# Optimization experiments

Hardware: AMD Instinct MI355X
Metric: run time of the kernel (lower is better)

The kernel has to match this reference:

```python
import jax, jax.numpy as jnp
import numpy as np
from jax import lax

N, S, C, D1, D2, P = 16384, 4096, 3, 256, 256, 16
MLP = [256, 256]
IN_CH = D1 + D2
K = 3
BIG = 1e8
EPS = 1e-8
BN_EPS = 1e-5


def setup_inputs() -> dict:
    key = jax.random.key(0)
    ks = jax.random.split(key, 16)
    inp = {
        'xyz1': jax.random.normal(ks[0], (1, C, N), jnp.float32),
        'xyz2': jax.random.normal(ks[1], (1, C, S), jnp.float32),
        'piece_id1': jax.random.randint(ks[2], (1, 1, N), 0, P, jnp.int64),
        'piece_id2': jax.random.randint(ks[3], (1, 1, S), 0, P, jnp.int64),
        'points1': jax.random.normal(ks[4], (1, D1, N), jnp.float32),
        'points2': jax.random.normal(ks[5], (1, D2, S), jnp.float32),
    }
    last = IN_CH
    for i, out in enumerate(MLP):
        inp[f'w{i}'] = jax.random.normal(ks[6 + 2 * i], (out, last), jnp.float32) / np.sqrt(last)
        inp[f'b{i}'] = jnp.zeros((out,), jnp.float32)
        inp[f'g{i}'] = jnp.ones((out,), jnp.float32)
        inp[f'bt{i}'] = jnp.zeros((out,), jnp.float32)
        last = out
    return inp


def _interpolate(xyz1, xyz2, pid1, pid2, points2):
    # xyz1 [1,3,N], xyz2 [1,3,S], pid [1,1,N]/[1,1,S], points2 [1,D,S]
    p1 = xyz1[0].T          # [N,3]
    p2 = xyz2[0].T          # [S,3]
    id1 = pid1[0, 0]        # [N]
    id2 = pid2[0, 0]        # [S]
    # squared euclidean distances, masked to same-piece neighbors (knn with batch vectors)
    d = jnp.sum((p1[:, None, :] - p2[None, :, :]) ** 2, axis=-1)  # [N,S]
    d = jnp.where(id1[:, None] != id2[None, :], jnp.inf, d)
    neg_d3, idx = lax.top_k(-d, K)    # 3 nearest per query
    d3 = -neg_d3                      # [N,3]
    valid = jnp.isfinite(d3)
    # missing neighbors -> reuse first idx with huge distance (fill_value semantics)
    idx = jnp.where(valid, idx, idx[:, :1])
    d3 = jnp.where(valid, d3, BIG)
    w = 1.0 / (d3 + EPS)
    w = w / jnp.sum(w, axis=-1, keepdims=True)   # [N,3]
    f2 = points2[0].T                            # [S,D2]
    interp = jnp.sum(f2[idx] * w[..., None], axis=1)  # [N,D2]
    return interp


def reference(xyz1, xyz2, piece_id1, piece_id2, points1, points2,
              w0, b0, g0, bt0, w1, b1, g1, bt1):
    interp = _interpolate(xyz1, xyz2, piece_id1, piece_id2, points2)  # [N,D2]
    feats = jnp.concatenate([points1[0].T, interp], axis=-1)          # [N,Cin]
    x = feats.T[None]                                                  # [1,Cin,N]
    for (wc, bc, g, bt) in ((w0, b0, g0, bt0), (w1, b1, g1, bt1)):
        y = jnp.einsum('oc,bcn->bon', wc, x) + bc[None, :, None]
        mean = jnp.mean(y, axis=(0, 2), keepdims=True)
        var = jnp.mean((y - mean) ** 2, axis=(0, 2), keepdims=True)
        y = (y - mean) * lax.rsqrt(var + BN_EPS)
        y = y * g[None, :, None] + bt[None, :, None]
        x = jax.nn.relu(y)
    return x
```

## Files before the change

### kernel.cpp

```cpp
#include <hip/hip_runtime.h>
#include <math.h>

#define NQ 16384
#define NS 4096
#define NCH 256
#define NP 16
#define BIGD 1e8f
#define EPSW 1e-8f

typedef __attribute__((ext_vector_type(8))) short short8;
typedef __attribute__((ext_vector_type(4))) float f32x4;

static __device__ __forceinline__ unsigned short f2bf(float x) {
    unsigned u = __float_as_uint(x);
    unsigned r = (u + 0x7fff + ((u >> 16) & 1)) >> 16;
    return (unsigned short)r;
}
static __device__ __forceinline__ float bf2f(unsigned short u) {
    return __uint_as_float(((unsigned)u) << 16);
}

__global__ __launch_bounds__(1024)
void bucket_kernel(const float* __restrict__ xyz2, const int* __restrict__ pid2,
                   float4* __restrict__ bpts, int* __restrict__ boff,
                   float* __restrict__ sums)
{
    __shared__ int spid[NS];
    __shared__ int segcnt[64][NP];
    __shared__ int segbase[64][NP];
    __shared__ int poff[NP + 1];
    const int t = threadIdx.x;
    sums[t] = 0.f;
    for (int i = t; i < NS; i += 1024) spid[i] = pid2[i];
    __syncthreads();
    {
        const int seg = t >> 4, p = t & 15;
        int c = 0;
        const int b = seg * 64;
        for (int i = 0; i < 64; ++i) c += (spid[b + i] == p);
        segcnt[seg][p] = c;
    }
    __syncthreads();
    if (t < NP) {
        int run = 0;
        for (int s = 0; s < 64; ++s) { segbase[s][t] = run; run += segcnt[s][t]; }
        poff[t] = run;
    }
    __syncthreads();
    if (t == 0) {
        int run = 0;
        for (int p = 0; p < NP; ++p) { int c = poff[p]; poff[p] = run; run += c; }
        poff[NP] = run;
    }
    __syncthreads();
    if (t <= NP) boff[t] = poff[t];
    {
        const int seg = t >> 4, p = t & 15;
        int pos = poff[p] + segbase[seg][p];
        const int b = seg * 64;
        for (int i = 0; i < 64; ++i) {
            const int gi = b + i;
            if (spid[gi] == p) {
                bpts[pos] = make_float4(xyz2[gi], xyz2[NS + gi], xyz2[2 * NS + gi],
                                        __int_as_float(gi));
                ++pos;
            }
        }
    }
}

#define LEXLT(d, j, e, je) ((d) < (e) || ((d) == (e) && (j) < (je)))

__global__ __launch_bounds__(256)
void knn_kernel(const float* __restrict__ xyz1, const int* __restrict__ pid1,
                const float4* __restrict__ bpts, const int* __restrict__ boff,
                int* __restrict__ oidx, float* __restrict__ ow)
{
    const int t = blockIdx.x * 256 + threadIdx.x;
    const int q = t >> 4;
    const int k = t & 15;
    const float qx = xyz1[q], qy = xyz1[NQ + q], qz = xyz1[2 * NQ + q];
    const int p = pid1[q];
    const int s0 = boff[p], s1 = boff[p + 1];

    float e0 = INFINITY, e1 = INFINITY, e2 = INFINITY;
    int j0 = 0, j1 = 0, j2 = 0;
    for (int i = s0 + k; i < s1; i += 16) {
        float4 pt = bpts[i];
        const float dx = pt.x - qx, dy = pt.y - qy, dz = pt.z - qz;
        const float d = fmaf(dx, dx, fmaf(dy, dy, dz * dz));
        const int oi = __float_as_int(pt.w);
        const bool b0 = LEXLT(d, oi, e0, j0), b1 = LEXLT(d, oi, e1, j1),
                   b2 = LEXLT(d, oi, e2, j2);
        e2 = b2 ? (b1 ? e1 : d) : e2;  j2 = b2 ? (b1 ? j1 : oi) : j2;
        e1 = b1 ? (b0 ? e0 : d) : e1;  j1 = b1 ? (b0 ? j0 : oi) : j1;
        e0 = b0 ? d : e0;              j0 = b0 ? oi : j0;
    }
    #pragma unroll
    for (int m = 1; m <= 8; m <<= 1) {
        float f[3]; int gi[3];
        f[0] = __shfl_xor(e0, m); gi[0] = __shfl_xor(j0, m);
        f[1] = __shfl_xor(e1, m); gi[1] = __shfl_xor(j1, m);
        f[2] = __shfl_xor(e2, m); gi[2] = __shfl_xor(j2, m);
        #pragma unroll
        for (int c = 0; c < 3; ++c) {
            const float d = f[c]; const int oi = gi[c];
            const bool b0 = LEXLT(d, oi, e0, j0), b1 = LEXLT(d, oi, e1, j1),
                       b2 = LEXLT(d, oi, e2, j2);
            e2 = b2 ? (b1 ? e1 : d) : e2;  j2 = b2 ? (b1 ? j1 : oi) : j2;
            e1 = b1 ? (b0 ? e0 : d) : e1;  j1 = b1 ? (b0 ? j0 : oi) : j1;
            e0 = b0 ? d : e0;              j0 = b0 ? oi : j0;
        }
    }
    if (k == 0) {
        if (isinf(e0)) { j0 = 0;  e0 = BIGD; }
        if (isinf(e1)) { j1 = j0; e1 = BIGD; }
        if (isinf(e2)) { j2 = j0; e2 = BIGD; }
        const float w0 = 1.f / (e0 + EPSW), w1 = 1.f / (e1 + EPSW), w2 = 1.f / (e2 + EPSW);
        const float inv = 1.f / (w0 + w1 + w2);
        oidx[q * 3 + 0] = j0; oidx[q * 3 + 1] = j1; oidx[q * 3 + 2] = j2;
        ow[q * 3 + 0] = w0 * inv; ow[q * 3 + 1] = w1 * inv; ow[q * 3 + 2] = w2 * inv;
    }
}

static __device__ __forceinline__
void tcvt_body(const float* __restrict__ src, int srcN,
               unsigned short* __restrict__ dst, int kt,
               int cb, int nb, float (*tile)[65])
{
    const int t = threadIdx.x;
    #pragma unroll
    for (int rnd = 0; rnd < 4; ++rnd) {
        const int r = rnd * 16 + (t >> 4);
        const int c4 = (t & 15) * 4;
        float4 v = *(const float4*)&src[(size_t)(cb + r) * srcN + nb + c4];
        tile[r][c4 + 0] = v.x; tile[r][c4 + 1] = v.y;
        tile[r][c4 + 2] = v.z; tile[r][c4 + 3] = v.w;
    }
    __syncthreads();
    #pragma unroll
    for (int half = 0; half < 2; ++half) {
        const int p  = (t >> 3) + half * 32;
        const int cg = t & 7;
        ushort4 o0, o1;
        o0.x = f2bf(tile[cg * 8 + 0][p]); o0.y = f2bf(tile[cg * 8 + 1][p]);
        o0.z = f2bf(tile[cg * 8 + 2][p]); o0.w = f2bf(tile[cg * 8 + 3][p]);
        o1.x = f2bf(tile[cg * 8 + 4][p]); o1.y = f2bf(tile[cg * 8 + 5][p]);
        o1.z = f2bf(tile[cg * 8 + 6][p]); o1.w = f2bf(tile[cg * 8 + 7][p]);
        ushort4* d = (ushort4*)&dst[(size_t)(nb + p) * kt + cb + cg * 8];
        d[0] = o0; d[1] = o1;
    }
}

static __device__ __forceinline__
void wrelay_body(const float* __restrict__ src, unsigned short* __restrict__ dst,
                 int K, int kslog, int o4)
{
    const int e4 = o4 & 1;
    const int tmp = o4 >> 1;
    const int l = tmp & 63;
    const int gks = tmp >> 6;
    const int ks = gks & ((1 << kslog) - 1);
    const int g  = gks >> kslog;
    const int row = g * 16 + (l & 15);
    const int col = ks * 32 + (l >> 4) * 8 + e4 * 4;
    float4 v = *(const float4*)&src[(size_t)row * K + col];
    ushort4 o;
    o.x = f2bf(v.x); o.y = f2bf(v.y); o.z = f2bf(v.z); o.w = f2bf(v.w);
    ((ushort4*)dst)[o4] = o;
}

__global__ __launch_bounds__(256)
void prep_kernel(const float* __restrict__ points1, const float* __restrict__ points2,
                 const float* __restrict__ w0, const float* __restrict__ w1,
                 unsigned short* __restrict__ Xt, unsigned short* __restrict__ p2Tb,
                 unsigned short* __restrict__ Wf0, unsigned short* __restrict__ Wf1)
{
    __shared__ float tile[64][65];
    const int b = blockIdx.x;
    if (b < 1024) {
        tcvt_body(points1, NQ, Xt, 512, (b & 3) * 64, (b >> 2) * 64, tile);
    } else if (b < 1280) {
        const int bb = b - 1024;
        tcvt_body(points2, NS, p2Tb, 256, (bb & 3) * 64, (bb >> 2) * 64, tile);
    } else if (b < 1408) {
        wrelay_body(w0, Wf0, 512, 4, (b - 1280) * 256 + threadIdx.x);
    } else {
        wrelay_body(w1, Wf1, 256, 3, (b - 1408) * 256 + threadIdx.x);
    }
}

__global__ __launch_bounds__(256)
void interp_kernel(const unsigned short* __restrict__ p2Tb,
                   const int* __restrict__ oidx, const float* __restrict__ ow,
                   unsigned short* __restrict__ Xt)
{
    const int n = (blockIdx.x * 256 + threadIdx.x) >> 6;
    const int l = threadIdx.x & 63;
    const int i0 = oidx[n * 3 + 0], i1 = oidx[n * 3 + 1], i2 = oidx[n * 3 + 2];
    const float w0 = ow[n * 3 + 0], w1 = ow[n * 3 + 1], w2 = ow[n * 3 + 2];
    ushort4 a = *(const ushort4*)&p2Tb[(size_t)i0 * 256 + l * 4];
    ushort4 b = *(const ushort4*)&p2Tb[(size_t)i1 * 256 + l * 4];
    ushort4 c = *(const ushort4*)&p2Tb[(size_t)i2 * 256 + l * 4];
    ushort4 o;
    o.x = f2bf(w0 * bf2f(a.x) + w1 * bf2f(b.x) + w2 * bf2f(c.x));
    o.y = f2bf(w0 * bf2f(a.y) + w1 * bf2f(b.y) + w2 * bf2f(c.y));
    o.z = f2bf(w0 * bf2f(a.z) + w1 * bf2f(b.z) + w2 * bf2f(c.z));
    o.w = f2bf(w0 * bf2f(a.w) + w1 * bf2f(b.w) + w2 * bf2f(c.w));
    *(ushort4*)&Xt[(size_t)n * 512 + 256 + l * 4] = o;
}

template<int K, bool LOAD_DIRECT>
__global__ __launch_bounds__(512)
void mgemm_kernel(const unsigned short* __restrict__ Wf,
                  const unsigned short* __restrict__ Xsrc,
                  const float* __restrict__ sum_in, const float* __restrict__ sq_in,
                  const float* __restrict__ g, const float* __restrict__ bt,
                  unsigned short* __restrict__ Yout)
{
    constexpr int K2 = K * 2;
    constexpr int KS = K / 32;
    __shared__ unsigned char sB[32 * K2];
    const int tid = threadIdx.x;
    const int n0 = blockIdx.x * 32;

    if constexpr (!LOAD_DIRECT) {
        __shared__ float scs[256], shs[256];
        if (tid < 256) {
            const float mean = sum_in[tid] * (1.f / NQ);
            const float var  = sq_in[tid] * (1.f / NQ) - mean * mean;
            const float rs = rsqrtf(var + 1e-5f);
            const float s = g[tid] * rs;
            scs[tid] = s; shs[tid] = bt[tid] - mean * s;
        }
        __syncthreads();
        const int row = tid >> 4;
        #pragma unroll
        for (int ch = 0; ch < 2; ++ch) {
            const int cb = (tid & 15) * 32 + ch * 16;
            const int c = cb / 2;
            const short8 v = *(const short8*)&Xsrc[(size_t)(n0 + row) * 256 + c];
            const float4 s0 = *(const float4*)&scs[c],     s1 = *(const float4*)&scs[c + 4];
            const float4 h0 = *(const float4*)&shs[c],     h1 = *(const float4*)&shs[c + 4];
            ushort4 lo, hi;
            lo.x = f2bf(fmaxf(fmaf(bf2f((unsigned short)v[0]), s0.x, h0.x), 0.f));
            lo.y = f2bf(fmaxf(fmaf(bf2f((unsigned short)v[1]), s0.y, h0.y), 0.f));
            lo.z = f2bf(fmaxf(fmaf(bf2f((unsigned short)v[2]), s0.z, h0.z), 0.f));
            lo.w = f2bf(fmaxf(fmaf(bf2f((unsigned short)v[3]), s0.w, h0.w), 0.f));
            hi.x = f2bf(fmaxf(fmaf(bf2f((unsigned short)v[4]), s1.x, h1.x), 0.f));
            hi.y = f2bf(fmaxf(fmaf(bf2f((unsigned short)v[5]), s1.y, h1.y), 0.f));
            hi.z = f2bf(fmaxf(fmaf(bf2f((unsigned short)v[6]), s1.z, h1.z), 0.f));
            hi.w = f2bf(fmaxf(fmaf(bf2f((unsigned short)v[7]), s1.w, h1.w), 0.f));
            unsigned char* d = &sB[row * K2 + (cb ^ ((row & 7) << 4))];
            ((ushort4*)d)[0] = lo; ((ushort4*)d)[1] = hi;
        }
    } else {
        constexpr int ROUNDS = (32 * K2 / 16) / 512;
        #pragma unroll
        for (int j = 0; j < ROUNDS; ++j) {
            const int p   = (j * 512 + tid) * 16;
            const int row = p >> 10;
            const int c   = p & (K2 - 1);
            const int q   = c ^ ((row & 7) << 4);
            const char* gp = (const char*)(Xsrc + (size_t)(n0 + row) * K) + q;
            __builtin_amdgcn_global_load_lds(
                (const __attribute__((address_space(1))) void*)gp,
                (__attribute__((address_space(3))) void*)(sB + p), 16, 0, 0);
        }
    }
    __syncthreads();

    const int w = tid >> 6, l = tid & 63;
    const int lr = l & 15, lk = l >> 4;
    f32x4 acc[2][2] = {};
    #pragma unroll
    for (int ks = 0; ks < KS; ++ks) {
        short8 b[2];
        #pragma unroll
        for (int nf = 0; nf < 2; ++nf) {
            const int r = nf * 16 + lr;
            const int cbyte = ks * 64 + lk * 16;
            b[nf] = *(const short8*)&sB[r * K2 + (cbyte ^ ((r & 7) << 4))];
        }
        #pragma unroll
        for (int mf = 0; mf < 2; ++mf) {
            const short8 a = *(const short8*)(
                Wf + (((size_t)(w * 2 + mf) * KS + ks) * 64 + l) * 8);
            #pragma unroll
            for (int nf = 0; nf < 2; ++nf)
                acc[mf][nf] = __builtin_amdgcn_mfma_f32_16x16x32_bf16(
                                  a, b[nf], acc[mf][nf], 0, 0, 0);
        }
    }
    #pragma unroll
    for (int mf = 0; mf < 2; ++mf)
        #pragma unroll
        for (int nf = 0; nf < 2; ++nf) {
            const int n = n0 + nf * 16 + lr;
            const int moff = w * 32 + mf * 16 + lk * 4;
            ushort4 o;
            o.x = f2bf(acc[mf][nf][0]); o.y = f2bf(acc[mf][nf][1]);
            o.z = f2bf(acc[mf][nf][2]); o.w = f2bf(acc[mf][nf][3]);
            *(ushort4*)&Yout[(size_t)n * 256 + moff] = o;
        }
}

__global__ __launch_bounds__(256)
void stats_kernel(const unsigned short* __restrict__ Y,
                  float* __restrict__ sum, float* __restrict__ sq)
{
    __shared__ float red[2][8][256];
    const int t = threadIdx.x;
    const int c8 = (t & 31) * 8;
    const int rsub = t >> 5;
    const int r0 = blockIdx.x * 256 + rsub;
    float s[8] = {}, q[8] = {};
    for (int i = 0; i < 32; ++i) {
        const short8 v = *(const short8*)&Y[(size_t)(r0 + i * 8) * 256 + c8];
        #pragma unroll
        for (int j = 0; j < 8; ++j) {
            const float f = bf2f((unsigned short)v[j]);
            s[j] += f; q[j] += f * f;
        }
    }
    #pragma unroll
    for (int j = 0; j < 8; ++j) {
        red[0][rsub][c8 + j] = s[j];
        red[1][rsub][c8 + j] = q[j];
    }
    __syncthreads();
    float ts = 0.f, tq = 0.f;
    #pragma unroll
    for (int r = 0; r < 8; ++r) { ts += red[0][r][t]; tq += red[1][r][t]; }
    atomicAdd(&sum[t], ts);
    atomicAdd(&sq[t], tq);
}

__global__ __launch_bounds__(256)
void bnt_kernel(const unsigned short* __restrict__ Y, const float* __restrict__ sum,
                const float* __restrict__ sq, const float* __restrict__ g,
                const float* __restrict__ bt, float* __restrict__ out)
{
    __shared__ float tile[64][65];
    __shared__ float scs[64], shs[64];
    const int t = threadIdx.x;
    const int cb = blockIdx.x * 64;
    const int nb = blockIdx.y * 64;
    if (t < 64) {
        const int c = cb + t;
        const float mean = sum[c] * (1.f / NQ);
        const float var  = sq[c] * (1.f / NQ) - mean * mean;
        const float rs = rsqrtf(var + 1e-5f);
        const float s = g[c] * rs;
        scs[t] = s; shs[t] = bt[c] - mean * s;
    }
    __syncthreads();
    #pragma unroll
    for (int rnd = 0; rnd < 4; ++rnd) {
        const int nl = rnd * 16 + (t >> 4);
        const int c4 = (t & 15) * 4;
        ushort4 v = *(const ushort4*)&Y[(size_t)(nb + nl) * 256 + cb + c4];
        tile[c4 + 0][nl] = fmaxf(fmaf(bf2f(v.x), scs[c4 + 0], shs[c4 + 0]), 0.f);
        tile[c4 + 1][nl] = fmaxf(fmaf(bf2f(v.y), scs[c4 + 1], shs[c4 + 1]), 0.f);
        tile[c4 + 2][nl] = fmaxf(fmaf(bf2f(v.z), scs[c4 + 2], shs[c4 + 2]), 0.f);
        tile[c4 + 3][nl] = fmaxf(fmaf(bf2f(v.w), scs[c4 + 3], shs[c4 + 3]), 0.f);
    }
    __syncthreads();
    const int cl = t >> 2, qq = t & 3;
    float* orow = out + (size_t)(cb + cl) * NQ + nb + qq * 16;
    #pragma unroll
    for (int k = 0; k < 4; ++k) {
        float4 v = make_float4(tile[cl][qq * 16 + k * 4 + 0], tile[cl][qq * 16 + k * 4 + 1],
                               tile[cl][qq * 16 + k * 4 + 2], tile[cl][qq * 16 + k * 4 + 3]);
        *(float4*)&orow[k * 4] = v;
    }
}

extern "C" void kernel_launch(void* const* d_in, const int* in_sizes, int n_in,
                              void* d_out, int out_size, void* d_ws, size_t ws_size,
                              hipStream_t stream)
{
    const float* xyz1    = (const float*)d_in[0];
    const float* xyz2    = (const float*)d_in[1];
    const int*   pid1    = (const int*)d_in[2];
    const int*   pid2    = (const int*)d_in[3];
    const float* points1 = (const float*)d_in[4];
    const float* points2 = (const float*)d_in[5];
    const float* w0      = (const float*)d_in[6];
    const float* g0      = (const float*)d_in[8];
    const float* bt0     = (const float*)d_in[9];
    const float* w1      = (const float*)d_in[10];
    const float* g1      = (const float*)d_in[12];
    const float* bt1     = (const float*)d_in[13];
    float* out = (float*)d_out;

    char* ws = (char*)d_ws;
    int*            boff  = (int*)(ws + 0);
    float*          sums  = (float*)(ws + 128);
    float*          sum0  = sums, *sq0 = sums + 256, *sum1 = sums + 512, *sq1 = sums + 768;
    int*            idxb  = (int*)(ws + 8192);
    float*          wb    = (float*)(ws + 8192 + 196608);
    unsigned short* Wf0   = (unsigned short*)(ws + 8192 + 393216);
    unsigned short* Wf1   = (unsigned short*)(ws + 8192 + 655360);
    float4*         bpts  = (float4*)(ws + 8192 + 786432);
    unsigned short* p2Tb  = (unsigned short*)(ws + 1048576);
    unsigned short* Xt    = (unsigned short*)(ws + 1048576 + 2097152);
    unsigned short* y0Tb  = (unsigned short*)(ws + 1048576 + 2097152 + 16777216);
    unsigned short* y1Tb  = (unsigned short*)(ws + 1048576 + 2097152 + 25165824);

    bucket_kernel<<<1, 1024, 0, stream>>>(xyz2, pid2, bpts, boff, sums);
    knn_kernel<<<NQ * 16 / 256, 256, 0, stream>>>(xyz1, pid1, bpts, boff, idxb, wb);
    prep_kernel<<<1472, 256, 0, stream>>>(points1, points2, w0, w1, Xt, p2Tb, Wf0, Wf1);
    interp_kernel<<<NQ * 64 / 256, 256, 0, stream>>>(p2Tb, idxb, wb, Xt);
    mgemm_kernel<512, true><<<NQ / 32, 512, 0, stream>>>(
        Wf0, Xt, nullptr, nullptr, nullptr, nullptr, y0Tb);
    stats_kernel<<<64, 256, 0, stream>>>(y0Tb, sum0, sq0);
    mgemm_kernel<256, false><<<NQ / 32, 512, 0, stream>>>(
        Wf1, y0Tb, sum0, sq0, g0, bt0, y1Tb);
    stats_kernel<<<64, 256, 0, stream>>>(y1Tb, sum1, sq1);
    bnt_kernel<<<dim3(4, NQ / 64), 256, 0, stream>>>(y1Tb, sum1, sq1, g1, bt1, out);
}
```

Before: 176.5 us.

## Fuse points1 transpose and interpolation into GEMM1, fold BN stats into GEMM epilogues

The first GEMM kernel now transposes and converts points1 to bf16 and computes the 3-NN weighted interpolation straight into LDS, so the Xt staging buffer and the separate interp pass are gone. Both GEMM kernels stage their output tile in swizzled LDS, write it out coalesced, and emit per-block channel sums and sums of squares. A small reduction kernel then turns these into BN scale and shift, replacing the atomic stats kernels that re-read Y. This removes several full-tensor global round trips and launches. The cost is more LDS per block and the loss of the async global-to-LDS load path in GEMM1.

```diff
diff --git a/kernel.cpp b/kernel.cpp
--- a/kernel.cpp
+++ b/kernel.cpp
@@ -3,7 +3,6 @@
 
 #define NQ 16384
 #define NS 4096
-#define NCH 256
 #define NP 16
 #define BIGD 1e8f
 #define EPSW 1e-8f
@@ -22,15 +21,13 @@
 
 __global__ __launch_bounds__(1024)
 void bucket_kernel(const float* __restrict__ xyz2, const int* __restrict__ pid2,
-                   float4* __restrict__ bpts, int* __restrict__ boff,
-                   float* __restrict__ sums)
+                   float4* __restrict__ bpts, int* __restrict__ boff)
 {
     __shared__ int spid[NS];
     __shared__ int segcnt[64][NP];
     __shared__ int segbase[64][NP];
     __shared__ int poff[NP + 1];
     const int t = threadIdx.x;
-    sums[t] = 0.f;
     for (int i = t; i < NS; i += 1024) spid[i] = pid2[i];
     __syncthreads();
     {
@@ -124,35 +121,6 @@
 }
 
 static __device__ __forceinline__
-void tcvt_body(const float* __restrict__ src, int srcN,
-               unsigned short* __restrict__ dst, int kt,
-               int cb, int nb, float (*tile)[65])
-{
-    const int t = threadIdx.x;
-    #pragma unroll
-    for (int rnd = 0; rnd < 4; ++rnd) {
-        const int r = rnd * 16 + (t >> 4);
-        const int c4 = (t & 15) * 4;
-        float4 v = *(const float4*)&src[(size_t)(cb + r) * srcN + nb + c4];
-        tile[r][c4 + 0] = v.x; tile[r][c4 + 1] = v.y;
-        tile[r][c4 + 2] = v.z; tile[r][c4 + 3] = v.w;
-    }
-    __syncthreads();
-    #pragma unroll
-    for (int half = 0; half < 2; ++half) {
-        const int p  = (t >> 3) + half * 32;
-        const int cg = t & 7;
-        ushort4 o0, o1;
-        o0.x = f2bf(tile[cg * 8 + 0][p]); o0.y = f2bf(tile[cg * 8 + 1][p]);
-        o0.z = f2bf(tile[cg * 8 + 2][p]); o0.w = f2bf(tile[cg * 8 + 3][p]);
-        o1.x = f2bf(tile[cg * 8 + 4][p]); o1.y = f2bf(tile[cg * 8 + 5][p]);
-        o1.z = f2bf(tile[cg * 8 + 6][p]); o1.w = f2bf(tile[cg * 8 + 7][p]);
-        ushort4* d = (ushort4*)&dst[(size_t)(nb + p) * kt + cb + cg * 8];
-        d[0] = o0; d[1] = o1;
-    }
-}
-
-static __device__ __forceinline__
 void wrelay_body(const float* __restrict__ src, unsigned short* __restrict__ dst,
                  int K, int kslog, int o4)
 {
@@ -171,189 +139,294 @@
 }
 
 __global__ __launch_bounds__(256)
-void prep_kernel(const float* __restrict__ points1, const float* __restrict__ points2,
+void prep_kernel(const float* __restrict__ points2,
                  const float* __restrict__ w0, const float* __restrict__ w1,
-                 unsigned short* __restrict__ Xt, unsigned short* __restrict__ p2Tb,
+                 unsigned short* __restrict__ p2Tb,
                  unsigned short* __restrict__ Wf0, unsigned short* __restrict__ Wf1)
 {
     __shared__ float tile[64][65];
-    const int b = blockIdx.x;
-    if (b < 1024) {
-        tcvt_body(points1, NQ, Xt, 512, (b & 3) * 64, (b >> 2) * 64, tile);
-    } else if (b < 1280) {
-        const int bb = b - 1024;
-        tcvt_body(points2, NS, p2Tb, 256, (bb & 3) * 64, (bb >> 2) * 64, tile);
-    } else if (b < 1408) {
-        wrelay_body(w0, Wf0, 512, 4, (b - 1280) * 256 + threadIdx.x);
+    const int b = blockIdx.x, t = threadIdx.x;
+    if (b < 256) {
+        const int cb = (b & 3) * 64, nb = (b >> 2) * 64;
+        #pragma unroll
+        for (int rnd = 0; rnd < 4; ++rnd) {
+            const int r = rnd * 16 + (t >> 4);
+            const int c4 = (t & 15) * 4;
+            float4 v = *(const float4*)&points2[(size_t)(cb + r) * NS + nb + c4];
+            tile[r][c4 + 0] = v.x; tile[r][c4 + 1] = v.y;
+            tile[r][c4 + 2] = v.z; tile[r][c4 + 3] = v.w;
+        }
+        __syncthreads();
+        #pragma unroll
+        for (int half = 0; half < 2; ++half) {
+            const int p  = (t >> 3) + half * 32;
+            const int cg = t & 7;
+            ushort4 o0, o1;
+            o0.x = f2bf(tile[cg*8+0][p]); o0.y = f2bf(tile[cg*8+1][p]);
+            o0.z = f2bf(tile[cg*8+2][p]); o0.w = f2bf(tile[cg*8+3][p]);
+            o1.x = f2bf(tile[cg*8+4][p]); o1.y = f2bf(tile[cg*8+5][p]);
+            o1.z = f2bf(tile[cg*8+6][p]); o1.w = f2bf(tile[cg*8+7][p]);
+            ushort4* d = (ushort4*)&p2Tb[(size_t)(nb + p) * 256 + cb + cg * 8];
+            d[0] = o0; d[1] = o1;
+        }
+    } else if (b < 384) {
+        wrelay_body(w0, Wf0, 512, 4, (b - 256) * 256 + t);
     } else {
-        wrelay_body(w1, Wf1, 256, 3, (b - 1408) * 256 + threadIdx.x);
-    }
-}
-
-__global__ __launch_bounds__(256)
-void interp_kernel(const unsigned short* __restrict__ p2Tb,
-                   const int* __restrict__ oidx, const float* __restrict__ ow,
-                   unsigned short* __restrict__ Xt)
-{
-    const int n = (blockIdx.x * 256 + threadIdx.x) >> 6;
-    const int l = threadIdx.x & 63;
-    const int i0 = oidx[n * 3 + 0], i1 = oidx[n * 3 + 1], i2 = oidx[n * 3 + 2];
-    const float w0 = ow[n * 3 + 0], w1 = ow[n * 3 + 1], w2 = ow[n * 3 + 2];
-    ushort4 a = *(const ushort4*)&p2Tb[(size_t)i0 * 256 + l * 4];
-    ushort4 b = *(const ushort4*)&p2Tb[(size_t)i1 * 256 + l * 4];
-    ushort4 c = *(const ushort4*)&p2Tb[(size_t)i2 * 256 + l * 4];
-    ushort4 o;
-    o.x = f2bf(w0 * bf2f(a.x) + w1 * bf2f(b.x) + w2 * bf2f(c.x));
-    o.y = f2bf(w0 * bf2f(a.y) + w1 * bf2f(b.y) + w2 * bf2f(c.y));
-    o.z = f2bf(w0 * bf2f(a.z) + w1 * bf2f(b.z) + w2 * bf2f(c.z));
-    o.w = f2bf(w0 * bf2f(a.w) + w1 * bf2f(b.w) + w2 * bf2f(c.w));
-    *(ushort4*)&Xt[(size_t)n * 512 + 256 + l * 4] = o;
-}
-
-template<int K, bool LOAD_DIRECT>
-__global__ __launch_bounds__(512)
-void mgemm_kernel(const unsigned short* __restrict__ Wf,
-                  const unsigned short* __restrict__ Xsrc,
-                  const float* __restrict__ sum_in, const float* __restrict__ sq_in,
-                  const float* __restrict__ g, const float* __restrict__ bt,
-                  unsigned short* __restrict__ Yout)
-{
-    constexpr int K2 = K * 2;
-    constexpr int KS = K / 32;
-    __shared__ unsigned char sB[32 * K2];
-    const int tid = threadIdx.x;
-    const int n0 = blockIdx.x * 32;
-
-    if constexpr (!LOAD_DIRECT) {
-        __shared__ float scs[256], shs[256];
-        if (tid < 256) {
-            const float mean = sum_in[tid] * (1.f / NQ);
-            const float var  = sq_in[tid] * (1.f / NQ) - mean * mean;
-            const float rs = rsqrtf(var + 1e-5f);
-            const float s = g[tid] * rs;
-            scs[tid] = s; shs[tid] = bt[tid] - mean * s;
-        }
-        __syncthreads();
-        const int row = tid >> 4;
-        #pragma unroll
-        for (int ch = 0; ch < 2; ++ch) {
-            const int cb = (tid & 15) * 32 + ch * 16;
-            const int c = cb / 2;
-            const short8 v = *(const short8*)&Xsrc[(size_t)(n0 + row) * 256 + c];
-            const float4 s0 = *(const float4*)&scs[c],     s1 = *(const float4*)&scs[c + 4];
-            const float4 h0 = *(const float4*)&shs[c],     h1 = *(const float4*)&shs[c + 4];
+        wrelay_body(w1, Wf1, 256, 3, (b - 384) * 256 + t);
+    }
+}
+
+__global__ __launch_bounds__(512, 4)
+void mgemm1f_kernel(const float* __restrict__ points1,
+                    const unsigned short* __restrict__ p2Tb,
+                    const int* __restrict__ idxb, const float* __restrict__ wb,
+                    const unsigned short* __restrict__ Wf0,
+                    unsigned short* __restrict__ y0Tb,
+                    float* __restrict__ psum, float* __restrict__ psq)
+{
+    __shared__ unsigned char sX[32768];
+    __shared__ unsigned char scratch[16896];
+    const int b = blockIdx.x, t = threadIdx.x;
+    const int n0 = b * 32;
+
+    {
+        float (*ft)[33] = (float(*)[33])scratch;
+        const int j = t & 31, cr = t >> 5;
+        for (int h = 0; h < 2; ++h) {
+            #pragma unroll
+            for (int i = 0; i < 8; ++i)
+                ft[cr + 16 * i][j] =
+                    points1[(size_t)(128 * h + cr + 16 * i) * NQ + n0 + j];
+            __syncthreads();
+            const int n = t >> 4, cc = t & 15;
             ushort4 lo, hi;
-            lo.x = f2bf(fmaxf(fmaf(bf2f((unsigned short)v[0]), s0.x, h0.x), 0.f));
-            lo.y = f2bf(fmaxf(fmaf(bf2f((unsigned short)v[1]), s0.y, h0.y), 0.f));
-            lo.z = f2bf(fmaxf(fmaf(bf2f((unsigned short)v[2]), s0.z, h0.z), 0.f));
-            lo.w = f2bf(fmaxf(fmaf(bf2f((unsigned short)v[3]), s0.w, h0.w), 0.f));
-            hi.x = f2bf(fmaxf(fmaf(bf2f((unsigned short)v[4]), s1.x, h1.x), 0.f));
-            hi.y = f2bf(fmaxf(fmaf(bf2f((unsigned short)v[5]), s1.y, h1.y), 0.f));
-            hi.z = f2bf(fmaxf(fmaf(bf2f((unsigned short)v[6]), s1.z, h1.z), 0.f));
-            hi.w = f2bf(fmaxf(fmaf(bf2f((unsigned short)v[7]), s1.w, h1.w), 0.f));
-            unsigned char* d = &sB[row * K2 + (cb ^ ((row & 7) << 4))];
+            lo.x = f2bf(ft[cc*8+0][n]); lo.y = f2bf(ft[cc*8+1][n]);
+            lo.z = f2bf(ft[cc*8+2][n]); lo.w = f2bf(ft[cc*8+3][n]);
+            hi.x = f2bf(ft[cc*8+4][n]); hi.y = f2bf(ft[cc*8+5][n]);
+            hi.z = f2bf(ft[cc*8+6][n]); hi.w = f2bf(ft[cc*8+7][n]);
+            const int cbyt = h * 256 + cc * 16;
+            unsigned char* d = &sX[n * 1024 + (cbyt ^ ((n & 7) << 4))];
             ((ushort4*)d)[0] = lo; ((ushort4*)d)[1] = hi;
-        }
-    } else {
-        constexpr int ROUNDS = (32 * K2 / 16) / 512;
-        #pragma unroll
-        for (int j = 0; j < ROUNDS; ++j) {
-            const int p   = (j * 512 + tid) * 16;
-            const int row = p >> 10;
-            const int c   = p & (K2 - 1);
-            const int q   = c ^ ((row & 7) << 4);
-            const char* gp = (const char*)(Xsrc + (size_t)(n0 + row) * K) + q;
-            __builtin_amdgcn_global_load_lds(
-                (const __attribute__((address_space(1))) void*)gp,
-                (__attribute__((address_space(3))) void*)(sB + p), 16, 0, 0);
-        }
-    }
-    __syncthreads();
-
-    const int w = tid >> 6, l = tid & 63;
-    const int lr = l & 15, lk = l >> 4;
+            __syncthreads();
+        }
+    }
+    {
+        const int n = t >> 4, cc = t & 15;
+        const int q = n0 + n;
+        const int i0 = idxb[q*3+0], i1 = idxb[q*3+1], i2 = idxb[q*3+2];
+        const float wa = wb[q*3+0], wv = wb[q*3+1], wc2 = wb[q*3+2];
+        const int ch0 = cc * 16;
+        const short8 A0 = *(const short8*)&p2Tb[(size_t)i0 * 256 + ch0];
+        const short8 A1 = *(const short8*)&p2Tb[(size_t)i0 * 256 + ch0 + 8];
+        const short8 B0 = *(const short8*)&p2Tb[(size_t)i1 * 256 + ch0];
+        const short8 B1 = *(const short8*)&p2Tb[(size_t)i1 * 256 + ch0 + 8];
+        const short8 C0 = *(const short8*)&p2Tb[(size_t)i2 * 256 + ch0];
+        const short8 C1 = *(const short8*)&p2Tb[(size_t)i2 * 256 + ch0 + 8];
+        unsigned short us[16];
+        #pragma unroll
+        for (int e = 0; e < 8; ++e) {
+            us[e]     = f2bf(wa * bf2f((unsigned short)A0[e]) +
+                             wv * bf2f((unsigned short)B0[e]) +
+                             wc2 * bf2f((unsigned short)C0[e]));
+            us[8 + e] = f2bf(wa * bf2f((unsigned short)A1[e]) +
+                             wv * bf2f((unsigned short)B1[e]) +
+                             wc2 * bf2f((unsigned short)C1[e]));
+        }
+        const int cb1 = 512 + cc * 32;
+        unsigned char* d0 = &sX[n * 1024 + (cb1 ^ ((n & 7) << 4))];
+        ((ushort4*)d0)[0] = make_ushort4(us[0], us[1], us[2], us[3]);
+        ((ushort4*)d0)[1] = make_ushort4(us[4], us[5], us[6], us[7]);
+        unsigned char* d1 = &sX[n * 1024 + ((cb1 + 16) ^ ((n & 7) << 4))];
+        ((ushort4*)d1)[0] = make_ushort4(us[8], us[9], us[10], us[11]);
+        ((ushort4*)d1)[1] = make_ushort4(us[12], us[13], us[14], us[15]);
+    }
+    __syncthreads();
+
+    const int w = t >> 6, l = t & 63, lr = l & 15, lk = l >> 4;
     f32x4 acc[2][2] = {};
     #pragma unroll
-    for (int ks = 0; ks < KS; ++ks) {
-        short8 b[2];
+    for (int ks = 0; ks < 16; ++ks) {
+        short8 bfv[2];
         #pragma unroll
         for (int nf = 0; nf < 2; ++nf) {
             const int r = nf * 16 + lr;
             const int cbyte = ks * 64 + lk * 16;
-            b[nf] = *(const short8*)&sB[r * K2 + (cbyte ^ ((r & 7) << 4))];
+            bfv[nf] = *(const short8*)&sX[r * 1024 + (cbyte ^ ((r & 7) << 4))];
         }
         #pragma unroll
         for (int mf = 0; mf < 2; ++mf) {
             const short8 a = *(const short8*)(
-                Wf + (((size_t)(w * 2 + mf) * KS + ks) * 64 + l) * 8);
+                Wf0 + (((size_t)(w * 2 + mf) * 16 + ks) * 64 + l) * 8);
             #pragma unroll
             for (int nf = 0; nf < 2; ++nf)
                 acc[mf][nf] = __builtin_amdgcn_mfma_f32_16x16x32_bf16(
-                                  a, b[nf], acc[mf][nf], 0, 0, 0);
-        }
-    }
+                                  a, bfv[nf], acc[mf][nf], 0, 0, 0);
+        }
+    }
+    __syncthreads();
+
+    unsigned char* yt = scratch;
     #pragma unroll
     for (int mf = 0; mf < 2; ++mf)
         #pragma unroll
         for (int nf = 0; nf < 2; ++nf) {
-            const int n = n0 + nf * 16 + lr;
-            const int moff = w * 32 + mf * 16 + lk * 4;
+            const int m = w * 32 + mf * 16 + lk * 4;
+            const int n = nf * 16 + lr;
             ushort4 o;
             o.x = f2bf(acc[mf][nf][0]); o.y = f2bf(acc[mf][nf][1]);
             o.z = f2bf(acc[mf][nf][2]); o.w = f2bf(acc[mf][nf][3]);
-            *(ushort4*)&Yout[(size_t)n * 256 + moff] = o;
-        }
+            *(ushort4*)&yt[n * 512 + ((m * 2) ^ ((n & 7) << 4))] = o;
+        }
+    __syncthreads();
+    {
+        const int n = t >> 4, cB = (t & 15) * 32;
+        ushort4 v0a = *(ushort4*)&yt[n * 512 + ((cB)      ^ ((n & 7) << 4))];
+        ushort4 v0b = *(ushort4*)&yt[n * 512 + ((cB + 8)  ^ ((n & 7) << 4))];
+        ushort4 v1a = *(ushort4*)&yt[n * 512 + ((cB + 16) ^ ((n & 7) << 4))];
+        ushort4 v1b = *(ushort4*)&yt[n * 512 + ((cB + 24) ^ ((n & 7) << 4))];
+        ushort4* dst = (ushort4*)&y0Tb[(size_t)(n0 + n) * 256 + (t & 15) * 16];
+        dst[0] = v0a; dst[1] = v0b; dst[2] = v1a; dst[3] = v1b;
+    }
+    if (t < 256) {
+        float s = 0.f, q = 0.f;
+        #pragma unroll 8
+        for (int n = 0; n < 32; ++n) {
+            const float f = bf2f(*(const unsigned short*)
+                &yt[n * 512 + ((t * 2) ^ ((n & 7) << 4))]);
+            s += f; q += f * f;
+        }
+        psum[b * 256 + t] = s; psq[b * 256 + t] = q;
+    }
 }
 
 __global__ __launch_bounds__(256)
-void stats_kernel(const unsigned short* __restrict__ Y,
-                  float* __restrict__ sum, float* __restrict__ sq)
-{
-    __shared__ float red[2][8][256];
-    const int t = threadIdx.x;
-    const int c8 = (t & 31) * 8;
-    const int rsub = t >> 5;
-    const int r0 = blockIdx.x * 256 + rsub;
-    float s[8] = {}, q[8] = {};
-    for (int i = 0; i < 32; ++i) {
-        const short8 v = *(const short8*)&Y[(size_t)(r0 + i * 8) * 256 + c8];
-        #pragma unroll
-        for (int j = 0; j < 8; ++j) {
-            const float f = bf2f((unsigned short)v[j]);
-            s[j] += f; q[j] += f * f;
-        }
-    }
-    #pragma unroll
-    for (int j = 0; j < 8; ++j) {
-        red[0][rsub][c8 + j] = s[j];
-        red[1][rsub][c8 + j] = q[j];
-    }
-    __syncthreads();
-    float ts = 0.f, tq = 0.f;
-    #pragma unroll
-    for (int r = 0; r < 8; ++r) { ts += red[0][r][t]; tq += red[1][r][t]; }
-    atomicAdd(&sum[t], ts);
-    atomicAdd(&sq[t], tq);
+void red_kernel(const float* __restrict__ psum, const float* __restrict__ psq,
+                const float* __restrict__ g, const float* __restrict__ bt,
+                float* __restrict__ gsc, float* __restrict__ gsh)
+{
+    const int c = blockIdx.x, t = threadIdx.x;
+    float s = psum[(size_t)t * 256 + c] + psum[(size_t)(t + 256) * 256 + c];
+    float q = psq [(size_t)t * 256 + c] + psq [(size_t)(t + 256) * 256 + c];
+    #pragma unroll
+    for (int off = 32; off; off >>= 1) {
+        s += __shfl_down(s, off); q += __shfl_down(q, off);
+    }
+    __shared__ float sr[4], qr[4];
+    if ((t & 63) == 0) { sr[t >> 6] = s; qr[t >> 6] = q; }
+    __syncthreads();
+    if (t == 0) {
+        float S = sr[0] + sr[1] + sr[2] + sr[3];
+        float Q = qr[0] + qr[1] + qr[2] + qr[3];
+        const float mean = S * (1.f / NQ);
+        const float var  = Q * (1.f / NQ) - mean * mean;
+        const float rs = rsqrtf(var + 1e-5f);
+        const float sc = g[c] * rs;
+        gsc[c] = sc; gsh[c] = bt[c] - mean * sc;
+    }
+}
+
+__global__ __launch_bounds__(512, 4)
+void mgemm2f_kernel(const unsigned short* __restrict__ Wf1,
+                    const unsigned short* __restrict__ y0Tb,
+                    const float* __restrict__ gsc, const float* __restrict__ gsh,
+                    unsigned short* __restrict__ y1Tb,
+                    float* __restrict__ psum, float* __restrict__ psq)
+{
+    __shared__ unsigned char sB[32 * 512];
+    __shared__ unsigned char yts[16384];
+    __shared__ float scs[256], shs[256];
+    const int b = blockIdx.x, t = threadIdx.x;
+    const int n0 = b * 32;
+    if (t < 256) { scs[t] = gsc[t]; shs[t] = gsh[t]; }
+    __syncthreads();
+    {
+        const int row = t >> 4;
+        const int ch0 = (t & 15) * 16;
+        const short8 v0 = *(const short8*)&y0Tb[(size_t)(n0 + row) * 256 + ch0];
+        const short8 v1 = *(const short8*)&y0Tb[(size_t)(n0 + row) * 256 + ch0 + 8];
+        unsigned short us[16];
+        #pragma unroll
+        for (int e = 0; e < 8; ++e) {
+            us[e]     = f2bf(fmaxf(fmaf(bf2f((unsigned short)v0[e]),
+                                        scs[ch0 + e], shs[ch0 + e]), 0.f));
+            us[8 + e] = f2bf(fmaxf(fmaf(bf2f((unsigned short)v1[e]),
+                                        scs[ch0 + 8 + e], shs[ch0 + 8 + e]), 0.f));
+        }
+        const int cb0 = ch0 * 2;
+        unsigned char* d0 = &sB[row * 512 + (cb0 ^ ((row & 7) << 4))];
+        ((ushort4*)d0)[0] = make_ushort4(us[0], us[1], us[2], us[3]);
+        ((ushort4*)d0)[1] = make_ushort4(us[4], us[5], us[6], us[7]);
+        unsigned char* d1 = &sB[row * 512 + ((cb0 + 16) ^ ((row & 7) << 4))];
+        ((ushort4*)d1)[0] = make_ushort4(us[8], us[9], us[10], us[11]);
+        ((ushort4*)d1)[1] = make_ushort4(us[12], us[13], us[14], us[15]);
+    }
+    __syncthreads();
+
+    const int w = t >> 6, l = t & 63, lr = l & 15, lk = l >> 4;
+    f32x4 acc[2][2] = {};
+    #pragma unroll
+    for (int ks = 0; ks < 8; ++ks) {
+        short8 bfv[2];
+        #pragma unroll
+        for (int nf = 0; nf < 2; ++nf) {
+            const int r = nf * 16 + lr;
+            const int cbyte = ks * 64 + lk * 16;
+            bfv[nf] = *(const short8*)&sB[r * 512 + (cbyte ^ ((r & 7) << 4))];
+        }
+        #pragma unroll
+        for (int mf = 0; mf < 2; ++mf) {
+            const short8 a = *(const short8*)(
+                Wf1 + (((size_t)(w * 2 + mf) * 8 + ks) * 64 + l) * 8);
+            #pragma unroll
+            for (int nf = 0; nf < 2; ++nf)
+                acc[mf][nf] = __builtin_amdgcn_mfma_f32_16x16x32_bf16(
+                                  a, bfv[nf], acc[mf][nf], 0, 0, 0);
+        }
+    }
+    unsigned char* yt = yts;
+    #pragma unroll
+    for (int mf = 0; mf < 2; ++mf)
+        #pragma unroll
+        for (int nf = 0; nf < 2; ++nf) {
+            const int m = w * 32 + mf * 16 + lk * 4;
+            const int n = nf * 16 + lr;
+            ushort4 o;
+            o.x = f2bf(acc[mf][nf][0]); o.y = f2bf(acc[mf][nf][1]);
+            o.z = f2bf(acc[mf][nf][2]); o.w = f2bf(acc[mf][nf][3]);
+            *(ushort4*)&yt[n * 512 + ((m * 2) ^ ((n & 7) << 4))] = o;
+        }
+    __syncthreads();
+    {
+        const int n = t >> 4, cB = (t & 15) * 32;
+        ushort4 v0a = *(ushort4*)&yt[n * 512 + ((cB)      ^ ((n & 7) << 4))];
+        ushort4 v0b = *(ushort4*)&yt[n * 512 + ((cB + 8)  ^ ((n & 7) << 4))];
+        ushort4 v1a = *(ushort4*)&yt[n * 512 + ((cB + 16) ^ ((n & 7) << 4))];
+        ushort4 v1b = *(ushort4*)&yt[n * 512 + ((cB + 24) ^ ((n & 7) << 4))];
+        ushort4* dst = (ushort4*)&y1Tb[(size_t)(n0 + n) * 256 + (t & 15) * 16];
+        dst[0] = v0a; dst[1] = v0b; dst[2] = v1a; dst[3] = v1b;
+    }
+    if (t < 256) {
+        float s = 0.f, q = 0.f;
+        #pragma unroll 8
+        for (int n = 0; n < 32; ++n) {
+            const float f = bf2f(*(const unsigned short*)
+                &yt[n * 512 + ((t * 2) ^ ((n & 7) << 4))]);
+            s += f; q += f * f;
+        }
+        psum[b * 256 + t] = s; psq[b * 256 + t] = q;
+    }
 }
 
 __global__ __launch_bounds__(256)
-void bnt_kernel(const unsigned short* __restrict__ Y, const float* __restrict__ sum,
-                const float* __restrict__ sq, const float* __restrict__ g,
-                const float* __restrict__ bt, float* __restrict__ out)
+void bnt_kernel(const unsigned short* __restrict__ Y, const float* __restrict__ gsc,
+                const float* __restrict__ gsh, float* __restrict__ out)
 {
     __shared__ float tile[64][65];
     __shared__ float scs[64], shs[64];
     const int t = threadIdx.x;
     const int cb = blockIdx.x * 64;
     const int nb = blockIdx.y * 64;
-    if (t < 64) {
-        const int c = cb + t;
-        const float mean = sum[c] * (1.f / NQ);
-        const float var  = sq[c] * (1.f / NQ) - mean * mean;
-        const float rs = rsqrtf(var + 1e-5f);
-        const float s = g[c] * rs;
-        scs[t] = s; shs[t] = bt[c] - mean * s;
-    }
+    if (t < 64) { scs[t] = gsc[cb + t]; shs[t] = gsh[cb + t]; }
     __syncthreads();
     #pragma unroll
     for (int rnd = 0; rnd < 4; ++rnd) {
@@ -396,27 +469,31 @@
 
     char* ws = (char*)d_ws;
     int*            boff  = (int*)(ws + 0);
-    float*          sums  = (float*)(ws + 128);
-    float*          sum0  = sums, *sq0 = sums + 256, *sum1 = sums + 512, *sq1 = sums + 768;
     int*            idxb  = (int*)(ws + 8192);
-    float*          wb    = (float*)(ws + 8192 + 196608);
-    unsigned short* Wf0   = (unsigned short*)(ws + 8192 + 393216);
-    unsigned short* Wf1   = (unsigned short*)(ws + 8192 + 655360);
-    float4*         bpts  = (float4*)(ws + 8192 + 786432);
-    unsigned short* p2Tb  = (unsigned short*)(ws + 1048576);
-    unsigned short* Xt    = (unsigned short*)(ws + 1048576 + 2097152);
-    unsigned short* y0Tb  = (unsigned short*)(ws + 1048576 + 2097152 + 16777216);
-    unsigned short* y1Tb  = (unsigned short*)(ws + 1048576 + 2097152 + 25165824);
-
-    bucket_kernel<<<1, 1024, 0, stream>>>(xyz2, pid2, bpts, boff, sums);
+    float*          wb    = (float*)(ws + 204800);
+    unsigned short* Wf0   = (unsigned short*)(ws + 401408);
+    unsigned short* Wf1   = (unsigned short*)(ws + 663552);
+    float4*         bpts  = (float4*)(ws + 794624);
+    float*          psum0 = (float*)(ws + 860160);
+    float*          psq0  = (float*)(ws + 1384448);
+    float*          psum1 = (float*)(ws + 1908736);
+    float*          psq1  = (float*)(ws + 2433024);
+    float*          gsc0  = (float*)(ws + 2957312);
+    float*          gsh0  = (float*)(ws + 2958336);
+    float*          gsc1  = (float*)(ws + 2959360);
+    float*          gsh1  = (float*)(ws + 2960384);
+    unsigned short* p2Tb  = (unsigned short*)(ws + 3145728);
+    unsigned short* y0Tb  = (unsigned short*)(ws + 5242880);
+    unsigned short* y1Tb  = (unsigned short*)(ws + 13631488);
+
+    bucket_kernel<<<1, 1024, 0, stream>>>(xyz2, pid2, bpts, boff);
     knn_kernel<<<NQ * 16 / 256, 256, 0, stream>>>(xyz1, pid1, bpts, boff, idxb, wb);
-    prep_kernel<<<1472, 256, 0, stream>>>(points1, points2, w0, w1, Xt, p2Tb, Wf0, Wf1);
-    interp_kernel<<<NQ * 64 / 256, 256, 0, stream>>>(p2Tb, idxb, wb, Xt);
-    mgemm_kernel<512, true><<<NQ / 32, 512, 0, stream>>>(
-        Wf0, Xt, nullptr, nullptr, nullptr, nullptr, y0Tb);
-    stats_kernel<<<64, 256, 0, stream>>>(y0Tb, sum0, sq0);
-    mgemm_kernel<256, false><<<NQ / 32, 512, 0, stream>>>(
-        Wf1, y0Tb, sum0, sq0, g0, bt0, y1Tb);
-    stats_kernel<<<64, 256, 0, stream>>>(y1Tb, sum1, sq1);
-    bnt_kernel<<<dim3(4, NQ / 64), 256, 0, stream>>>(y1Tb, sum1, sq1, g1, bt1, out);
-}
+    prep_kernel<<<448, 256, 0, stream>>>(points2, w0, w1, p2Tb, Wf0, Wf1);
+    mgemm1f_kernel<<<NQ / 32, 512, 0, stream>>>(points1, p2Tb, idxb, wb, Wf0,
+                                                y0Tb, psum0, psq0);
+    red_kernel<<<256, 256, 0, stream>>>(psum0, psq0, g0, bt0, gsc0, gsh0);
+    mgemm2f_kernel<<<NQ / 32, 512, 0, stream>>>(Wf1, y0Tb, gsc0, gsh0,
+                                                y1Tb, psum1, psq1);
+    red_kernel<<<256, 256, 0, stream>>>(psum1, psq1, g1, bt1, gsc1, gsh1);
+    bnt_kernel<<<dim3(4, NQ / 64), 256, 0, stream>>>(y1Tb, gsc1, gsh1, out);
+}
```

Measured after the change: 164.1 us. 7.0% less time.
